# Optimization experiments

Measured on AMD Instinct MI355X. Metric: run time of the kernel, lower is better.

Reference implementation:

```python
import jax, jax.numpy as jnp
import numpy as np

B, N, FD, HD, G = 32, 512, 768, 384, 3
ALPHA = 0.2  # LeakyReLU slope
NEG = -9e15


def layer_norm(x, g, b, eps=1e-5):
    m = jnp.mean(x, axis=-1, keepdims=True)
    v = jnp.var(x, axis=-1, keepdims=True)
    return (x - m) / jnp.sqrt(v + eps) * g + b


def gat_layer(x, adj, W, a):
    # x: [B,N,FD], adj: [N,N], W: [FD,HD], a: [2*HD]
    h = jnp.einsum('bnf,fd->bnd', x, W)  # [B,N,HD]
    # concat score decomposes: e_ij = lrelu(h_i . a[:HD] + h_j . a[HD:])
    e1 = h @ a[:HD]   # [B,N]
    e2 = h @ a[HD:]   # [B,N]
    e = jax.nn.leaky_relu(e1[:, :, None] + e2[:, None, :], ALPHA)  # [B,N,N]
    e = jnp.where(adj[None] > 0, e, NEG)
    att = jax.nn.softmax(e, axis=2)  # masked softmax over neighbors
    h_prime = jnp.einsum('bij,bjd->bid', att, h)
    return jax.nn.elu(h_prime)  # concat=True -> ELU


def setup_inputs() -> dict:
    key = jax.random.key(0)
    ks = jax.random.split(key, 10)
    s = 0.05
    return {
        'x': jax.random.normal(ks[0], (B, N, FD), jnp.float32),
        'adj': jax.random.randint(ks[1], (G, N, N), 0, 2),
        'W': jax.random.normal(ks[2], (G, FD, HD), jnp.float32) * s,
        'a': jax.random.normal(ks[3], (G, 2 * HD), jnp.float32) * s,
        'log_unc': jnp.zeros((G,), jnp.float32),
        'gate_w': jax.random.normal(ks[4], (FD, G), jnp.float32) * s,
        'gate_b': jnp.zeros((G,), jnp.float32),
        'ln1_g': jnp.ones((HD,), jnp.float32),
        'ln1_b': jnp.zeros((HD,), jnp.float32),
        'w1': jax.random.normal(ks[5], (HD, HD), jnp.float32) * s,
        'b1': jnp.zeros((HD,), jnp.float32),
        'w2': jax.random.normal(ks[6], (HD, FD), jnp.float32) * s,
        'b2': jnp.zeros((FD,), jnp.float32),
        'ln2_g': jnp.ones((FD,), jnp.float32),
        'ln2_b': jnp.zeros((FD,), jnp.float32),
    }


def reference(x, adj, W, a, log_unc, gate_w, gate_b, ln1_g, ln1_b,
              w1, b1, w2, b2, ln2_g, ln2_b):
    # global (uncertainty) weights
    unc = jnp.exp(log_unc)
    attw = jax.nn.softmax(1.0 / (unc + 1e-8))  # [G]
    # content gates from batch-averaged features
    avg = jnp.mean(x, axis=0)                          # [N,FD]
    cg = jax.nn.softmax(avg @ gate_w + gate_b, axis=-1)  # [N,G]
    # per-graph GAT + LayerNorm, vmapped over the G graphs
    gouts = jax.vmap(lambda ad, Wi, ai: layer_norm(gat_layer(x, ad, Wi, ai), ln1_g, ln1_b))(adj, W, a)  # [G,B,N,HD]
    weights = 0.7 * attw[:, None, None, None] + 0.3 * cg.T[:, None, :, None]  # [G,1|B,N,1]
    fused = jnp.sum(weights * gouts, axis=0)  # [B,N,HD]
    # output projection + LayerNorm
    proj = jax.nn.relu(fused @ w1 + b1) @ w2 + b2
    proj = layer_norm(proj, ln2_g, ln2_b)
    # residual gate
    gv = jax.nn.sigmoid(jnp.sum(proj * x, axis=-1, keepdims=True) / np.sqrt(FD).astype(np.float32))
    return gv * x + (1.0 - gv) * proj
```

## Files before the change

### kernel.cpp

```cpp
#include <hip/hip_runtime.h>

typedef unsigned short ushort_t;
typedef unsigned int uint_t;
typedef __bf16 bf16x8 __attribute__((ext_vector_type(8)));
typedef float f32x4 __attribute__((ext_vector_type(4)));
typedef unsigned int u32x4 __attribute__((ext_vector_type(4)));
typedef unsigned short u16x4 __attribute__((ext_vector_type(4)));

#define B_SZ 32
#define N_SZ 512
#define FD_SZ 768
#define HD_SZ 384
#define G_SZ 3
#define M_SZ (B_SZ * N_SZ)
#define ALPHA_LR 0.2f
#define NEGV -9.0e15f
#define VTILE (HD_SZ * 32)

__device__ __forceinline__ float bflo(uint_t u) { return __uint_as_float(u << 16); }
__device__ __forceinline__ float bfhi(uint_t u) { return __uint_as_float(u & 0xffff0000u); }
__device__ __forceinline__ float bf2f(ushort_t u) { return __uint_as_float(((uint_t)u) << 16); }
__device__ __forceinline__ ushort_t f2bf(float f) {
  uint_t x = __float_as_uint(f);
  return (ushort_t)((x + 0x7fffu + ((x >> 16) & 1u)) >> 16);
}
__device__ __forceinline__ u32x4 pack8(f32x4 lo, f32x4 hi) {
  union { ushort_t us[8]; u32x4 v; } pk;
  pk.us[0] = f2bf(lo.x); pk.us[1] = f2bf(lo.y); pk.us[2] = f2bf(lo.z); pk.us[3] = f2bf(lo.w);
  pk.us[4] = f2bf(hi.x); pk.us[5] = f2bf(hi.y); pk.us[6] = f2bf(hi.z); pk.us[7] = f2bf(hi.w);
  return pk.v;
}

__global__ __launch_bounds__(256) void transpose_f2b(
    const float* __restrict__ src, ushort_t* __restrict__ dst, int R, int C) {
  size_t total = (size_t)R * C;
  size_t base = (size_t)blockIdx.z * total;
  size_t i = (size_t)blockIdx.x * 256 + threadIdx.x;
  if (i < total) {
    int r = (int)(i / C), c = (int)(i % C);
    dst[base + (size_t)c * R + r] = f2bf(src[base + i]);
  }
}

__global__ __launch_bounds__(256) void pack_adj(
    const int* __restrict__ adj, uint_t* __restrict__ am) {
  size_t i = (size_t)blockIdx.x * 256 + threadIdx.x;
  unsigned long long mask = __ballot(adj[i] != 0);
  int lane = threadIdx.x & 63;
  if ((lane & 31) == 0) am[i >> 5] = (uint_t)(mask >> (lane & 32));
}

__global__ __launch_bounds__(256) void gate_kernel(
    const float* __restrict__ x, const float* __restrict__ gate_w,
    const float* __restrict__ gate_b, float* __restrict__ cg) {
  int n = blockIdx.x;
  int tid = threadIdx.x;
  float a0 = 0.f, a1 = 0.f, a2 = 0.f;
  for (int f = tid; f < FD_SZ; f += 256) {
    float s = 0.f;
#pragma unroll
    for (int b = 0; b < B_SZ; b++) s += x[((size_t)b * N_SZ + n) * FD_SZ + f];
    float avg = s * (1.0f / B_SZ);
    a0 += avg * gate_w[f * 3 + 0];
    a1 += avg * gate_w[f * 3 + 1];
    a2 += avg * gate_w[f * 3 + 2];
  }
  for (int m = 1; m < 64; m <<= 1) {
    a0 += __shfl_xor(a0, m, 64);
    a1 += __shfl_xor(a1, m, 64);
    a2 += __shfl_xor(a2, m, 64);
  }
  __shared__ float red[3][4];
  int wave = tid >> 6, lane = tid & 63;
  if (lane == 0) { red[0][wave] = a0; red[1][wave] = a1; red[2][wave] = a2; }
  __syncthreads();
  if (tid == 0) {
    float l0 = red[0][0] + red[0][1] + red[0][2] + red[0][3] + gate_b[0];
    float l1 = red[1][0] + red[1][1] + red[1][2] + red[1][3] + gate_b[1];
    float l2 = red[2][0] + red[2][1] + red[2][2] + red[2][3] + gate_b[2];
    float mx = fmaxf(l0, fmaxf(l1, l2));
    float e0 = __expf(l0 - mx), e1 = __expf(l1 - mx), e2 = __expf(l2 - mx);
    float inv = 1.0f / (e0 + e1 + e2);
    cg[n * 3 + 0] = e0 * inv;
    cg[n * 3 + 1] = e1 * inv;
    cg[n * 3 + 2] = e2 * inv;
  }
}

template <bool AF32, bool RELU, bool OUTBF16, bool HASBIAS, bool VFOUT>
__global__ __launch_bounds__(256) void gemm_kernel(
    const void* __restrict__ Av, size_t strideA,
    const ushort_t* __restrict__ Bt, size_t strideB,
    const float* __restrict__ bias,
    void* __restrict__ Cv, size_t strideC,
    int M, int K, int Nc) {
  __shared__ __attribute__((aligned(16))) ushort_t As[128 * 32];
  __shared__ __attribute__((aligned(16))) ushort_t Bs[128 * 32];
  int tid = threadIdx.x, wave = tid >> 6, lane = tid & 63;
  int m0 = blockIdx.y * 128, n0 = blockIdx.x * 128;
  const float* Abf32 = (const float*)Av + (size_t)blockIdx.z * strideA;
  const ushort_t* Abb16 = (const ushort_t*)Av + (size_t)blockIdx.z * strideA;
  const ushort_t* Bb = Bt + (size_t)blockIdx.z * strideB;

  f32x4 acc[4][4];
  f32x4 z4 = {0.f, 0.f, 0.f, 0.f};
#pragma unroll
  for (int i = 0; i < 4; i++)
#pragma unroll
    for (int j = 0; j < 4; j++) acc[i][j] = z4;

  int wm = (wave & 1) * 64, wn = (wave >> 1) * 64;
  int srow = lane >> 2, schk = (lane & 3) * 8;

  for (int kt = 0; kt < K; kt += 32) {
    u32x4 av[2], bv[2];
#pragma unroll
    for (int i = 0; i < 2; i++) {
      int row = m0 + wave * 32 + i * 16 + srow;
      if (AF32) {
        const float* ap = Abf32 + (size_t)row * K + kt + schk;
        f32x4 lo = *(const f32x4*)ap;
        f32x4 hi = *(const f32x4*)(ap + 4);
        av[i] = pack8(lo, hi);
      } else {
        av[i] = *(const u32x4*)(Abb16 + (size_t)row * K + kt + schk);
      }
      bv[i] = *(const u32x4*)(Bb + (size_t)(n0 + wave * 32 + i * 16 + srow) * K + kt + schk);
    }
    __syncthreads();
#pragma unroll
    for (int i = 0; i < 2; i++) {
      int rowBase = wave * 32 + i * 16;
      *(u32x4*)(As + rowBase * 32 + lane * 8) = av[i];
      *(u32x4*)(Bs + rowBase * 32 + lane * 8) = bv[i];
    }
    __syncthreads();
    bf16x8 af[4], bfr[4];
#pragma unroll
    for (int t = 0; t < 4; t++) {
      af[t] = *(const bf16x8*)(As + (wm + t * 16 + (lane & 15)) * 32 + (lane >> 4) * 8);
      bfr[t] = *(const bf16x8*)(Bs + (wn + t * 16 + (lane & 15)) * 32 + (lane >> 4) * 8);
    }
#pragma unroll
    for (int mt = 0; mt < 4; mt++)
#pragma unroll
      for (int nt = 0; nt < 4; nt++)
        acc[mt][nt] = __builtin_amdgcn_mfma_f32_16x16x32_bf16(af[mt], bfr[nt], acc[mt][nt], 0, 0, 0);
  }

  if (VFOUT) {
#pragma unroll
    for (int mt = 0; mt < 4; mt++) {
#pragma unroll
      for (int nt = 0; nt < 4; nt++) {
        int d = n0 + wn + nt * 16 + (lane & 15);
        int gm = m0 + wm + mt * 16 + (lane >> 4) * 4;
        int b = gm >> 9, jt = (gm >> 5) & 15, j2 = gm & 31;
        u16x4 pk;
#pragma unroll
        for (int r2 = 0; r2 < 4; r2++) pk[r2] = f2bf(acc[mt][nt][r2]);
        size_t off = ((size_t)((blockIdx.z * B_SZ + b) * 16 + jt)) * VTILE + (size_t)d * 32 + j2;
        *(u16x4*)((ushort_t*)Cv + off) = pk;
      }
    }
  } else {
#pragma unroll
    for (int mt = 0; mt < 4; mt++) {
#pragma unroll
      for (int nt = 0; nt < 4; nt++) {
        int gn = n0 + wn + nt * 16 + (lane & 15);
        float bvs = HASBIAS ? bias[gn] : 0.f;
#pragma unroll
        for (int r2 = 0; r2 < 4; r2++) {
          int gm = m0 + wm + mt * 16 + (lane >> 4) * 4 + r2;
          float v = acc[mt][nt][r2] + bvs;
          if (RELU) v = v > 0.f ? v : 0.f;
          size_t off = (size_t)blockIdx.z * strideC + (size_t)gm * Nc + gn;
          if (OUTBF16) ((ushort_t*)Cv)[off] = f2bf(v);
          else ((float*)Cv)[off] = v;
        }
      }
    }
  }
}

__global__ __launch_bounds__(256) void e12_kernel(
    const ushort_t* __restrict__ vf, const float* __restrict__ a,
    float* __restrict__ e1, float* __restrict__ e2) {
  __shared__ float a1s[HD_SZ], a2s[HD_SZ];
  int g = blockIdx.y;
  int tid = threadIdx.x;
  for (int i = tid; i < HD_SZ; i += 256) {
    a1s[i] = a[g * 2 * HD_SZ + i];
    a2s[i] = a[g * 2 * HD_SZ + HD_SZ + i];
  }
  __syncthreads();
  int m = blockIdx.x * 256 + tid;
  int b = m >> 9, jt = (m >> 5) & 15, j2 = m & 31;
  const ushort_t* col = vf + ((size_t)((g * B_SZ + b) * 16 + jt)) * VTILE + j2;
  float s1 = 0.f, s2 = 0.f;
  for (int d = 0; d < HD_SZ; d++) {
    float h = bf2f(col[d * 32]);
    s1 += h * a1s[d];
    s2 += h * a2s[d];
  }
  e1[(size_t)g * M_SZ + m] = s1;
  e2[(size_t)g * M_SZ + m] = s2;
}

__global__ __launch_bounds__(512, 4) void attn_kernel(
    const uint_t* __restrict__ adjm, const ushort_t* __restrict__ vf,
    const float* __restrict__ e1, const float* __restrict__ e2,
    const float* __restrict__ cg, const float* __restrict__ log_unc,
    const float* __restrict__ ln1g, const float* __restrict__ ln1b,
    ushort_t* __restrict__ fusedbf) {
  __shared__ __attribute__((aligned(16))) ushort_t Pb[16][520];
  __shared__ float e2s[512];
  __shared__ float e1r[16];
  __shared__ uint_t amS[16][16];
  __shared__ float lng[HD_SZ], lnb[HD_SZ];
  __shared__ float cgr[16][3];
  __shared__ float s1s[16][8], s2s[16][8];

  int tid = threadIdx.x, wave = tid >> 6, lane = tid & 63;
  int quad = lane >> 4, l15 = lane & 15;
  int L = blockIdx.x + (blockIdx.y << 5);
  int b = (L & 7) + ((L >> 8) << 3);
  int i0 = ((L >> 3) & 31) * 16;

  float iv0 = 1.f / (__expf(log_unc[0]) + 1e-8f);
  float iv1 = 1.f / (__expf(log_unc[1]) + 1e-8f);
  float iv2 = 1.f / (__expf(log_unc[2]) + 1e-8f);
  float mxa = fmaxf(iv0, fmaxf(iv1, iv2));
  float w0 = __expf(iv0 - mxa), w1 = __expf(iv1 - mxa), w2 = __expf(iv2 - mxa);
  float wsum = 1.f / (w0 + w1 + w2);
  float attw[3] = {w0 * wsum, w1 * wsum, w2 * wsum};

  for (int idx = tid; idx < HD_SZ; idx += 512) {
    lng[idx] = ln1g[idx];
    lnb[idx] = ln1b[idx];
  }
  if (tid < 48) cgr[tid / 3][tid % 3] = cg[(i0 + tid / 3) * 3 + tid % 3];

  float facc[12];
#pragma unroll
  for (int t = 0; t < 12; t++) facc[t] = 0.f;

  for (int g = 0; g < G_SZ; g++) {
    __syncthreads();
    if (tid < 16) e1r[tid] = e1[((size_t)g * B_SZ + b) * N_SZ + i0 + tid];
    if (tid < 256)
      amS[tid >> 4][tid & 15] = adjm[((size_t)g * N_SZ + i0 + (tid >> 4)) * 16 + (tid & 15)];
    for (int idx = tid; idx < N_SZ; idx += 512)
      e2s[idx] = e2[((size_t)g * B_SZ + b) * N_SZ + idx];
    __syncthreads();

#pragma unroll
    for (int rr = 0; rr < 2; rr++) {
      int rw = wave * 2 + rr;
      float e1v = e1r[rw];
      float sv[8];
      float m = -3.0e38f;
#pragma unroll
      for (int jj = 0; jj < 8; jj++) {
        int j = lane + jj * 64;
        float s = e1v + e2s[j];
        s = s > 0.f ? s : ALPHA_LR * s;
        uint_t mw = amS[rw][(lane >> 5) + jj * 2];
        s = ((mw >> (j & 31)) & 1u) ? s : NEGV;
        sv[jj] = s;
        m = fmaxf(m, s);
      }
      for (int msk = 1; msk < 64; msk <<= 1) m = fmaxf(m, __shfl_xor(m, msk, 64));
      float sum = 0.f;
#pragma unroll
      for (int jj = 0; jj < 8; jj++) {
        float e = __expf(sv[jj] - m);
        sv[jj] = e;
        sum += e;
      }
      for (int msk = 1; msk < 64; msk <<= 1) sum += __shfl_xor(sum, msk, 64);
      float inv = 1.0f / sum;
#pragma unroll
      for (int jj = 0; jj < 8; jj++) Pb[rw][lane + jj * 64] = f2bf(sv[jj] * inv);
    }
    __syncthreads();

    f32x4 acc[3];
    f32x4 z4 = {0.f, 0.f, 0.f, 0.f};
#pragma unroll
    for (int t = 0; t < 3; t++) acc[t] = z4;
    const ushort_t* vbase = vf + ((size_t)(g * B_SZ + b) * 16) * VTILE;
#pragma unroll 2
    for (int j0 = 0; j0 < N_SZ; j0 += 32) {
      bf16x8 af = *(const bf16x8*)(&Pb[l15][j0 + quad * 8]);
      const ushort_t* vtile = vbase + (size_t)(j0 >> 5) * VTILE;
#pragma unroll
      for (int t = 0; t < 3; t++) {
        bf16x8 bf = *(const bf16x8*)(vtile + (wave * 48 + t * 16 + l15) * 32 + quad * 8);
        acc[t] = __builtin_amdgcn_mfma_f32_16x16x32_bf16(af, bf, acc[t], 0, 0, 0);
      }
    }

    float o[12];
    float ps1[4] = {0.f, 0.f, 0.f, 0.f}, ps2[4] = {0.f, 0.f, 0.f, 0.f};
#pragma unroll
    for (int t = 0; t < 3; t++)
#pragma unroll
      for (int r = 0; r < 4; r++) {
        float v = acc[t][r];
        v = v > 0.f ? v : __expf(v) - 1.f;
        o[t * 4 + r] = v;
        ps1[r] += v;
        ps2[r] += v * v;
      }
#pragma unroll
    for (int msk = 1; msk < 16; msk <<= 1) {
#pragma unroll
      for (int r = 0; r < 4; r++) {
        ps1[r] += __shfl_xor(ps1[r], msk, 64);
        ps2[r] += __shfl_xor(ps2[r], msk, 64);
      }
    }
    if (l15 == 0) {
#pragma unroll
      for (int r = 0; r < 4; r++) {
        s1s[quad * 4 + r][wave] = ps1[r];
        s2s[quad * 4 + r][wave] = ps2[r];
      }
    }
    __syncthreads();
#pragma unroll
    for (int r = 0; r < 4; r++) {
      int row = quad * 4 + r;
      float S1 = 0.f, S2 = 0.f;
#pragma unroll
      for (int w = 0; w < 8; w++) {
        S1 += s1s[row][w];
        S2 += s2s[row][w];
      }
      float mean = S1 * (1.f / HD_SZ);
      float var = S2 * (1.f / HD_SZ) - mean * mean;
      float rs = rsqrtf(var + 1e-5f);
      float wgt = 0.7f * attw[g] + 0.3f * cgr[row][g];
#pragma unroll
      for (int t = 0; t < 3; t++) {
        int d = wave * 48 + t * 16 + l15;
        facc[t * 4 + r] += wgt * ((o[t * 4 + r] - mean) * rs * lng[d] + lnb[d]);
      }
    }
  }
#pragma unroll
  for (int r = 0; r < 4; r++) {
    size_t rowo = ((size_t)b * N_SZ + i0 + quad * 4 + r) * HD_SZ;
#pragma unroll
    for (int t = 0; t < 3; t++)
      fusedbf[rowo + wave * 48 + t * 16 + l15] = f2bf(facc[t * 4 + r]);
  }
}

__global__ __launch_bounds__(256) void final_kernel(
    const ushort_t* __restrict__ projbf, const float* __restrict__ x,
    const float* __restrict__ ln2g, const float* __restrict__ ln2b,
    float* __restrict__ out) {
  int row = blockIdx.x;
  int tid = threadIdx.x, wave = tid >> 6, lane = tid & 63;
  const ushort_t* pr = projbf + (size_t)row * FD_SZ;
  const float* xr = x + (size_t)row * FD_SZ;
  float v[3], xv[3];
  float s1 = 0.f, s2 = 0.f;
#pragma unroll
  for (int k = 0; k < 3; k++) {
    int c = tid + k * 256;
    v[k] = bf2f(pr[c]);
    xv[k] = xr[c];
    s1 += v[k];
    s2 += v[k] * v[k];
  }
  for (int m = 1; m < 64; m <<= 1) {
    s1 += __shfl_xor(s1, m, 64);
    s2 += __shfl_xor(s2, m, 64);
  }
  __shared__ float rs1[4], rs2[4], rdt[4];
  if (lane == 0) { rs1[wave] = s1; rs2[wave] = s2; }
  __syncthreads();
  s1 = rs1[0] + rs1[1] + rs1[2] + rs1[3];
  s2 = rs2[0] + rs2[1] + rs2[2] + rs2[3];
  float mean = s1 * (1.f / FD_SZ);
  float var = s2 * (1.f / FD_SZ) - mean * mean;
  float rstd = rsqrtf(var + 1e-5f);
  float dot = 0.f;
  float pn[3];
#pragma unroll
  for (int k = 0; k < 3; k++) {
    int c = tid + k * 256;
    pn[k] = (v[k] - mean) * rstd * ln2g[c] + ln2b[c];
    dot += pn[k] * xv[k];
  }
  for (int m = 1; m < 64; m <<= 1) dot += __shfl_xor(dot, m, 64);
  if (lane == 0) rdt[wave] = dot;
  __syncthreads();
  dot = rdt[0] + rdt[1] + rdt[2] + rdt[3];
  float gv = 1.f / (1.f + __expf(-dot * (1.0f / 27.712812921102035f)));
#pragma unroll
  for (int k = 0; k < 3; k++) {
    int c = tid + k * 256;
    out[(size_t)row * FD_SZ + c] = gv * xv[k] + (1.f - gv) * pn[k];
  }
}

extern "C" void kernel_launch(void* const* d_in, const int* in_sizes, int n_in,
                              void* d_out, int out_size, void* d_ws, size_t ws_size,
                              hipStream_t stream) {
  (void)in_sizes; (void)n_in; (void)out_size; (void)ws_size;
  const float* x = (const float*)d_in[0];
  const int* adj = (const int*)d_in[1];
  const float* W = (const float*)d_in[2];
  const float* a = (const float*)d_in[3];
  const float* log_unc = (const float*)d_in[4];
  const float* gate_w = (const float*)d_in[5];
  const float* gate_b = (const float*)d_in[6];
  const float* ln1g = (const float*)d_in[7];
  const float* ln1b = (const float*)d_in[8];
  const float* w1 = (const float*)d_in[9];
  const float* b1 = (const float*)d_in[10];
  const float* w2 = (const float*)d_in[11];
  const float* b2 = (const float*)d_in[12];
  const float* ln2g = (const float*)d_in[13];
  const float* ln2b = (const float*)d_in[14];

  char* ws = (char*)d_ws;
  ushort_t* Wt      = (ushort_t*)(ws + 0);
  uint_t*   adjm    = (uint_t*)(ws + 0);
  ushort_t* w1t     = (ushort_t*)(ws + 1769472);
  ushort_t* w2t     = (ushort_t*)(ws + 2064384);
  float*    cg      = (float*)(ws + 2654208);
  float*    e1      = (float*)(ws + 2660352);
  float*    e2      = (float*)(ws + 2856960);
  ushort_t* fusedbf = (ushort_t*)(ws + 3053568);
  ushort_t* vf      = (ushort_t*)(ws + 15636480);
  ushort_t* t1bf    = (ushort_t*)(ws + 15636480);
  ushort_t* projbf  = (ushort_t*)(ws + 28219392);

  transpose_f2b<<<dim3(1152, 1, 3), 256, 0, stream>>>(W, Wt, FD_SZ, HD_SZ);
  transpose_f2b<<<dim3(576, 1, 1), 256, 0, stream>>>(w1, w1t, HD_SZ, HD_SZ);
  transpose_f2b<<<dim3(1152, 1, 1), 256, 0, stream>>>(w2, w2t, HD_SZ, FD_SZ);

  gate_kernel<<<dim3(N_SZ), 256, 0, stream>>>(x, gate_w, gate_b, cg);

  gemm_kernel<true, false, true, false, true><<<dim3(3, 128, 3), 256, 0, stream>>>(
      x, 0, Wt, (size_t)HD_SZ * FD_SZ, nullptr, vf, 0,
      M_SZ, FD_SZ, HD_SZ);

  pack_adj<<<dim3((G_SZ * N_SZ * N_SZ) / 256), 256, 0, stream>>>(adj, adjm);

  e12_kernel<<<dim3(M_SZ / 256, G_SZ), 256, 0, stream>>>(vf, a, e1, e2);

  attn_kernel<<<dim3(N_SZ / 16, B_SZ), 512, 0, stream>>>(
      adjm, vf, e1, e2, cg, log_unc, ln1g, ln1b, fusedbf);

  gemm_kernel<false, true, true, true, false><<<dim3(3, 128, 1), 256, 0, stream>>>(
      fusedbf, 0, w1t, 0, b1, t1bf, 0, M_SZ, HD_SZ, HD_SZ);
  gemm_kernel<false, false, true, true, false><<<dim3(6, 128, 1), 256, 0, stream>>>(
      t1bf, 0, w2t, 0, b2, projbf, 0, M_SZ, HD_SZ, FD_SZ);

  final_kernel<<<dim3(M_SZ), 256, 0, stream>>>(projbf, x, ln2g, ln2b, (float*)d_out);
}
```

Measured before the change: 372.2 us.

## Process 32 query rows per attention block and pre-cast x to bf16 for GEMM

The attention kernel now handles 32 rows per block instead of 16, running two MFMA row tiles against each loaded V fragment. This halves the global reads of V per output row and halves the grid size. Separately, x is cast to bf16 once into the output buffer, which is reused as scratch, and the first GEMM reads bf16 rather than converting fp32 on the fly. The cost is an extra pass over x and higher register pressure from 24 accumulators plus 2x3 MFMA accumulators, which may reduce occupancy under launch_bounds(512,4).

```diff
diff --git a/kernel.cpp b/kernel.cpp
--- a/kernel.cpp
+++ b/kernel.cpp
@@ -17,8 +17,6 @@
 #define NEGV -9.0e15f
 #define VTILE (HD_SZ * 32)
 
-__device__ __forceinline__ float bflo(uint_t u) { return __uint_as_float(u << 16); }
-__device__ __forceinline__ float bfhi(uint_t u) { return __uint_as_float(u & 0xffff0000u); }
 __device__ __forceinline__ float bf2f(ushort_t u) { return __uint_as_float(((uint_t)u) << 16); }
 __device__ __forceinline__ ushort_t f2bf(float f) {
   uint_t x = __float_as_uint(f);
@@ -40,6 +38,15 @@
     int r = (int)(i / C), c = (int)(i % C);
     dst[base + (size_t)c * R + r] = f2bf(src[base + i]);
   }
+}
+
+__global__ __launch_bounds__(256) void cast_f2b(
+    const float* __restrict__ src, ushort_t* __restrict__ dst) {
+  size_t i = (size_t)blockIdx.x * 256 + threadIdx.x;
+  f32x4 v = ((const f32x4*)src)[i];
+  u16x4 p;
+  p[0] = f2bf(v.x); p[1] = f2bf(v.y); p[2] = f2bf(v.z); p[3] = f2bf(v.w);
+  ((u16x4*)dst)[i] = p;
 }
 
 __global__ __launch_bounds__(256) void pack_adj(
@@ -214,19 +221,19 @@
     const float* __restrict__ cg, const float* __restrict__ log_unc,
     const float* __restrict__ ln1g, const float* __restrict__ ln1b,
     ushort_t* __restrict__ fusedbf) {
-  __shared__ __attribute__((aligned(16))) ushort_t Pb[16][520];
+  __shared__ __attribute__((aligned(16))) ushort_t Pb[32][520];
   __shared__ float e2s[512];
-  __shared__ float e1r[16];
-  __shared__ uint_t amS[16][16];
+  __shared__ float e1r[32];
+  __shared__ uint_t amS[32][16];
   __shared__ float lng[HD_SZ], lnb[HD_SZ];
-  __shared__ float cgr[16][3];
-  __shared__ float s1s[16][8], s2s[16][8];
+  __shared__ float cgr[32][3];
+  __shared__ float s1s[32][8], s2s[32][8];
 
   int tid = threadIdx.x, wave = tid >> 6, lane = tid & 63;
   int quad = lane >> 4, l15 = lane & 15;
-  int L = blockIdx.x + (blockIdx.y << 5);
-  int b = (L & 7) + ((L >> 8) << 3);
-  int i0 = ((L >> 3) & 31) * 16;
+  int L = blockIdx.x + (blockIdx.y << 4);
+  int b = (L & 7) + ((L >> 7) << 3);
+  int i0 = ((L >> 3) & 15) * 32;
 
   float iv0 = 1.f / (__expf(log_unc[0]) + 1e-8f);
   float iv1 = 1.f / (__expf(log_unc[1]) + 1e-8f);
@@ -236,28 +243,26 @@
   float wsum = 1.f / (w0 + w1 + w2);
   float attw[3] = {w0 * wsum, w1 * wsum, w2 * wsum};
 
-  for (int idx = tid; idx < HD_SZ; idx += 512) {
-    lng[idx] = ln1g[idx];
-    lnb[idx] = ln1b[idx];
-  }
-  if (tid < 48) cgr[tid / 3][tid % 3] = cg[(i0 + tid / 3) * 3 + tid % 3];
-
-  float facc[12];
-#pragma unroll
-  for (int t = 0; t < 12; t++) facc[t] = 0.f;
+  if (tid < HD_SZ) {
+    lng[tid] = ln1g[tid];
+    lnb[tid] = ln1b[tid];
+  }
+  if (tid < 96) cgr[tid / 3][tid % 3] = cg[(i0 + tid / 3) * 3 + tid % 3];
+
+  float facc[24];
+#pragma unroll
+  for (int t = 0; t < 24; t++) facc[t] = 0.f;
 
   for (int g = 0; g < G_SZ; g++) {
     __syncthreads();
-    if (tid < 16) e1r[tid] = e1[((size_t)g * B_SZ + b) * N_SZ + i0 + tid];
-    if (tid < 256)
-      amS[tid >> 4][tid & 15] = adjm[((size_t)g * N_SZ + i0 + (tid >> 4)) * 16 + (tid & 15)];
-    for (int idx = tid; idx < N_SZ; idx += 512)
-      e2s[idx] = e2[((size_t)g * B_SZ + b) * N_SZ + idx];
-    __syncthreads();
-
-#pragma unroll
-    for (int rr = 0; rr < 2; rr++) {
-      int rw = wave * 2 + rr;
+    if (tid < 32) e1r[tid] = e1[((size_t)g * B_SZ + b) * N_SZ + i0 + tid];
+    amS[tid >> 4][tid & 15] = adjm[((size_t)g * N_SZ + i0 + (tid >> 4)) * 16 + (tid & 15)];
+    e2s[tid] = e2[((size_t)g * B_SZ + b) * N_SZ + tid];
+    __syncthreads();
+
+#pragma unroll
+    for (int rr = 0; rr < 4; rr++) {
+      int rw = wave * 4 + rr;
       float e1v = e1r[rw];
       float sv[8];
       float m = -3.0e38f;
@@ -286,77 +291,94 @@
     }
     __syncthreads();
 
-    f32x4 acc[3];
+    f32x4 acc[2][3];
     f32x4 z4 = {0.f, 0.f, 0.f, 0.f};
 #pragma unroll
-    for (int t = 0; t < 3; t++) acc[t] = z4;
+    for (int mt = 0; mt < 2; mt++)
+#pragma unroll
+      for (int t = 0; t < 3; t++) acc[mt][t] = z4;
     const ushort_t* vbase = vf + ((size_t)(g * B_SZ + b) * 16) * VTILE;
 #pragma unroll 2
     for (int j0 = 0; j0 < N_SZ; j0 += 32) {
-      bf16x8 af = *(const bf16x8*)(&Pb[l15][j0 + quad * 8]);
       const ushort_t* vtile = vbase + (size_t)(j0 >> 5) * VTILE;
+      bf16x8 af0 = *(const bf16x8*)(&Pb[l15][j0 + quad * 8]);
+      bf16x8 af1 = *(const bf16x8*)(&Pb[16 + l15][j0 + quad * 8]);
 #pragma unroll
       for (int t = 0; t < 3; t++) {
         bf16x8 bf = *(const bf16x8*)(vtile + (wave * 48 + t * 16 + l15) * 32 + quad * 8);
-        acc[t] = __builtin_amdgcn_mfma_f32_16x16x32_bf16(af, bf, acc[t], 0, 0, 0);
-      }
-    }
-
-    float o[12];
-    float ps1[4] = {0.f, 0.f, 0.f, 0.f}, ps2[4] = {0.f, 0.f, 0.f, 0.f};
-#pragma unroll
-    for (int t = 0; t < 3; t++)
+        acc[0][t] = __builtin_amdgcn_mfma_f32_16x16x32_bf16(af0, bf, acc[0][t], 0, 0, 0);
+        acc[1][t] = __builtin_amdgcn_mfma_f32_16x16x32_bf16(af1, bf, acc[1][t], 0, 0, 0);
+      }
+    }
+
+    float ps1[2][4], ps2[2][4];
+#pragma unroll
+    for (int mt = 0; mt < 2; mt++)
+#pragma unroll
+      for (int r = 0; r < 4; r++) { ps1[mt][r] = 0.f; ps2[mt][r] = 0.f; }
+#pragma unroll
+    for (int mt = 0; mt < 2; mt++)
+#pragma unroll
+      for (int t = 0; t < 3; t++)
+#pragma unroll
+        for (int r = 0; r < 4; r++) {
+          float v = acc[mt][t][r];
+          v = v > 0.f ? v : __expf(v) - 1.f;
+          acc[mt][t][r] = v;
+          ps1[mt][r] += v;
+          ps2[mt][r] += v * v;
+        }
+#pragma unroll
+    for (int msk = 1; msk < 16; msk <<= 1) {
+#pragma unroll
+      for (int mt = 0; mt < 2; mt++)
+#pragma unroll
+        for (int r = 0; r < 4; r++) {
+          ps1[mt][r] += __shfl_xor(ps1[mt][r], msk, 64);
+          ps2[mt][r] += __shfl_xor(ps2[mt][r], msk, 64);
+        }
+    }
+    if (l15 == 0) {
+#pragma unroll
+      for (int mt = 0; mt < 2; mt++)
+#pragma unroll
+        for (int r = 0; r < 4; r++) {
+          s1s[mt * 16 + quad * 4 + r][wave] = ps1[mt][r];
+          s2s[mt * 16 + quad * 4 + r][wave] = ps2[mt][r];
+        }
+    }
+    __syncthreads();
+#pragma unroll
+    for (int mt = 0; mt < 2; mt++)
 #pragma unroll
       for (int r = 0; r < 4; r++) {
-        float v = acc[t][r];
-        v = v > 0.f ? v : __expf(v) - 1.f;
-        o[t * 4 + r] = v;
-        ps1[r] += v;
-        ps2[r] += v * v;
-      }
-#pragma unroll
-    for (int msk = 1; msk < 16; msk <<= 1) {
-#pragma unroll
-      for (int r = 0; r < 4; r++) {
-        ps1[r] += __shfl_xor(ps1[r], msk, 64);
-        ps2[r] += __shfl_xor(ps2[r], msk, 64);
-      }
-    }
-    if (l15 == 0) {
-#pragma unroll
-      for (int r = 0; r < 4; r++) {
-        s1s[quad * 4 + r][wave] = ps1[r];
-        s2s[quad * 4 + r][wave] = ps2[r];
-      }
-    }
-    __syncthreads();
+        int row = mt * 16 + quad * 4 + r;
+        float S1 = 0.f, S2 = 0.f;
+#pragma unroll
+        for (int w = 0; w < 8; w++) {
+          S1 += s1s[row][w];
+          S2 += s2s[row][w];
+        }
+        float mean = S1 * (1.f / HD_SZ);
+        float var = S2 * (1.f / HD_SZ) - mean * mean;
+        float rs = rsqrtf(var + 1e-5f);
+        float wgt = 0.7f * attw[g] + 0.3f * cgr[row][g];
+#pragma unroll
+        for (int t = 0; t < 3; t++) {
+          int d = wave * 48 + t * 16 + l15;
+          facc[mt * 12 + t * 4 + r] += wgt * ((acc[mt][t][r] - mean) * rs * lng[d] + lnb[d]);
+        }
+      }
+  }
+#pragma unroll
+  for (int mt = 0; mt < 2; mt++)
 #pragma unroll
     for (int r = 0; r < 4; r++) {
-      int row = quad * 4 + r;
-      float S1 = 0.f, S2 = 0.f;
-#pragma unroll
-      for (int w = 0; w < 8; w++) {
-        S1 += s1s[row][w];
-        S2 += s2s[row][w];
-      }
-      float mean = S1 * (1.f / HD_SZ);
-      float var = S2 * (1.f / HD_SZ) - mean * mean;
-      float rs = rsqrtf(var + 1e-5f);
-      float wgt = 0.7f * attw[g] + 0.3f * cgr[row][g];
-#pragma unroll
-      for (int t = 0; t < 3; t++) {
-        int d = wave * 48 + t * 16 + l15;
-        facc[t * 4 + r] += wgt * ((o[t * 4 + r] - mean) * rs * lng[d] + lnb[d]);
-      }
-    }
-  }
-#pragma unroll
-  for (int r = 0; r < 4; r++) {
-    size_t rowo = ((size_t)b * N_SZ + i0 + quad * 4 + r) * HD_SZ;
-#pragma unroll
-    for (int t = 0; t < 3; t++)
-      fusedbf[rowo + wave * 48 + t * 16 + l15] = f2bf(facc[t * 4 + r]);
-  }
+      size_t rowo = ((size_t)b * N_SZ + i0 + mt * 16 + quad * 4 + r) * HD_SZ;
+#pragma unroll
+      for (int t = 0; t < 3; t++)
+        fusedbf[rowo + wave * 48 + t * 16 + l15] = f2bf(facc[mt * 12 + t * 4 + r]);
+    }
 }
 
 __global__ __launch_bounds__(256) void final_kernel(
@@ -441,6 +463,9 @@
   ushort_t* vf      = (ushort_t*)(ws + 15636480);
   ushort_t* t1bf    = (ushort_t*)(ws + 15636480);
   ushort_t* projbf  = (ushort_t*)(ws + 28219392);
+  ushort_t* xb      = (ushort_t*)d_out;
+
+  cast_f2b<<<dim3((M_SZ * FD_SZ) / 1024), 256, 0, stream>>>(x, xb);
 
   transpose_f2b<<<dim3(1152, 1, 3), 256, 0, stream>>>(W, Wt, FD_SZ, HD_SZ);
   transpose_f2b<<<dim3(576, 1, 1), 256, 0, stream>>>(w1, w1t, HD_SZ, HD_SZ);
@@ -448,15 +473,15 @@
 
   gate_kernel<<<dim3(N_SZ), 256, 0, stream>>>(x, gate_w, gate_b, cg);
 
-  gemm_kernel<true, false, true, false, true><<<dim3(3, 128, 3), 256, 0, stream>>>(
-      x, 0, Wt, (size_t)HD_SZ * FD_SZ, nullptr, vf, 0,
+  gemm_kernel<false, false, true, false, true><<<dim3(3, 128, 3), 256, 0, stream>>>(
+      xb, 0, Wt, (size_t)HD_SZ * FD_SZ, nullptr, vf, 0,
       M_SZ, FD_SZ, HD_SZ);
 
   pack_adj<<<dim3((G_SZ * N_SZ * N_SZ) / 256), 256, 0, stream>>>(adj, adjm);
 
   e12_kernel<<<dim3(M_SZ / 256, G_SZ), 256, 0, stream>>>(vf, a, e1, e2);
 
-  attn_kernel<<<dim3(N_SZ / 16, B_SZ), 512, 0, stream>>>(
+  attn_kernel<<<dim3(N_SZ / 32, B_SZ), 512, 0, stream>>>(
       adjm, vf, e1, e2, cg, log_unc, ln1g, ln1b, fusedbf);
 
   gemm_kernel<false, true, true, true, false><<<dim3(3, 128, 1), 256, 0, stream>>>(
```

After: 349.0 us. -6.2%, faster.
